# Kernel optimization log

Hardware: AMD Instinct MI355X
Metric: run time of the kernel (lower is better)

The kernel has to match this reference:

```python
import jax, jax.numpy as jnp
import numpy as np

BATCH, NUM_MASKS, IN_DIM, OUT_DIM = 512, 16, 1024, 1024


def setup_inputs() -> dict:
    key = jax.random.key(0)
    k1, k2, k3 = jax.random.split(key, 3)
    x = jax.random.normal(k1, (BATCH, NUM_MASKS, IN_DIM), dtype=jnp.float32)
    kernel = jax.random.normal(k2, (IN_DIM, OUT_DIM), dtype=jnp.float32) * (1.0 / np.sqrt(IN_DIM))
    masks = jax.random.uniform(k3, (NUM_MASKS, IN_DIM, OUT_DIM), dtype=jnp.float32)
    return {"x": x, "kernel": kernel, "masks": masks}


def reference(x, kernel, masks):
    # masked_kernel[m, i, o] = kernel[i, o] * masks[m, i, o]
    masked_kernel = kernel[None, :, :] * masks  # (M, I, O)
    # Original tf.scan serializes batch; equivalent math is one batched einsum:
    # out[b, m, o] = sum_i x[b, m, i] * masked_kernel[m, i, o]
    # NOTE: the executed tf.scan path applies NO activation, so neither do we.
    out = jnp.einsum('bmi,mio->bmo', x, masked_kernel)  # (B, M, O)
    return out
```

## Files before the change

kernel.cpp:

```cpp
#include <hip/hip_runtime.h>
#include <hip/hip_bf16.h>


#define BATCH 512
#define NMASK 16
#define IN_D  1024
#define OUT_D 1024

using bf16x8 = __attribute__((ext_vector_type(8))) __bf16;
using bf16x4 = __attribute__((ext_vector_type(4))) __bf16;
using f32x16 = __attribute__((ext_vector_type(16))) float;
using f32x4  = __attribute__((ext_vector_type(4))) float;
using f32x2  = __attribute__((ext_vector_type(2))) float;

typedef const __attribute__((address_space(1))) void gvoid_t;
typedef __attribute__((address_space(3))) void lvoid_t;

__device__ __forceinline__ void dma16(const void* g, const void* l) {
    __builtin_amdgcn_global_load_lds((gvoid_t*)(uintptr_t)g,
                                     (lvoid_t*)(uintptr_t)l, 16, 0, 0);
}

__global__ void __launch_bounds__(512, 4)
mdl_prep(const float* __restrict__ X,
         const float* __restrict__ Kn,
         const float* __restrict__ Mk,
         unsigned short* __restrict__ Wt,
         unsigned short* __restrict__ Xp)
{
    const int t   = threadIdx.x;
    const int bid = blockIdx.x;

    if (bid < 1024) {
        const int wg = (bid & 7) * 128 + (bid >> 3);
        const int m  = wg >> 6;
        const int G2 = wg & 63;
        const int g01 = t >> 8;
        const int oc  = t & 255;
        const int col0 = oc * 4;
        const int G = G2 * 2 + g01;
        const int i0 = G * 8;

        const float* mkb = Mk + ((size_t)m * IN_D + i0) * OUT_D + col0;
        const float* knb = Kn + (size_t)i0 * OUT_D + col0;

        f32x4 a[8], b[8];
#pragma unroll
        for (int r = 0; r < 8; ++r) {
            a[r] = *(const f32x4*)(mkb + (size_t)r * OUT_D);
            b[r] = *(const f32x4*)(knb + (size_t)r * OUT_D);
        }
        unsigned short* dst =
            Wt + (((size_t)m * 128 + G) * 1024 + col0) * 8;
#pragma unroll
        for (int c = 0; c < 4; ++c) {
            bf16x8 g;
#pragma unroll
            for (int r = 0; r < 8; ++r)
                g[r] = (__bf16)(a[r][c] * b[r][c]);
            *(bf16x8*)(dst + c * 8) = g;
        }
    } else {
        const int b2    = bid - 1024;
        const int strip = b2 >> 2;
        const int Gq    = b2 & 3;
        const int m  = strip >> 3;
        const int bt = strip & 7;
        const int row = t >> 3;
        const int oc  = t & 7;

        const float* src = X + ((size_t)(bt * 64 + row) * NMASK + m) * IN_D
                             + Gq * 256 + oc * 32;
        f32x4 av[8];
#pragma unroll
        for (int q = 0; q < 8; ++q)
            av[q] = *(const f32x4*)(src + q * 4);

        unsigned short* dstS = Xp + (size_t)strip * 65536
                                  + (size_t)(Gq * 32 + oc * 4) * 512 + row * 8;
#pragma unroll
        for (int j = 0; j < 4; ++j) {
            bf16x8 g;
#pragma unroll
            for (int e = 0; e < 4; ++e) {
                g[e]     = (__bf16)av[2 * j][e];
                g[4 + e] = (__bf16)av[2 * j + 1][e];
            }
            *(bf16x8*)(dstS + (size_t)j * 512) = g;
        }
    }
}

struct Frags { bf16x8 a[2][2]; bf16x8 b[2][2]; };

__global__ void __launch_bounds__(256, 2)
mdl_gemm2(const unsigned short* __restrict__ Xp,
          const unsigned short* __restrict__ Wt,
          float* __restrict__ Out)
{
    const int t = threadIdx.x;
    const int l = t & 63;
    const int w = t >> 6;

    const int raw = blockIdx.x;
    const int wg  = (raw & 7) * 64 + (raw >> 3);
    const int v   = wg * 4 + w;
    const int m   = v >> 7;
    const int v7  = v & 127;
    const int bt  = v7 >> 4;
    const int ot  = v7 & 15;

    const unsigned short* Ap = Xp + (size_t)(m * 8 + bt) * 65536;
    const int la = (l & 31) * 8;
    const int ls = l >> 5;
    const int bcol = ot * 64 + (l & 31);

    f32x16 acc[2][2];
#pragma unroll
    for (int ti = 0; ti < 2; ++ti)
#pragma unroll
        for (int tj = 0; tj < 2; ++tj)
#pragma unroll
            for (int e = 0; e < 16; ++e)
                acc[ti][tj][e] = 0.f;

    auto LOADF = [&](Frags& F, int kb) {
#pragma unroll
        for (int s = 0; s < 2; ++s) {
            const int G = (kb >> 3) + s * 2 + ls;
            const unsigned short* ab = Ap + (size_t)G * 512 + la;
            F.a[s][0] = *(const bf16x8*)(ab);
            F.a[s][1] = *(const bf16x8*)(ab + 256);
            const unsigned short* bb =
                Wt + (((size_t)m * 128 + G) * 1024 + bcol) * 8;
            F.b[s][0] = *(const bf16x8*)(bb);
            F.b[s][1] = *(const bf16x8*)(bb + 256);
        }
    };
    auto MF = [&](Frags& F) {
#pragma unroll
        for (int s = 0; s < 2; ++s)
#pragma unroll
            for (int ti = 0; ti < 2; ++ti)
#pragma unroll
                for (int tj = 0; tj < 2; ++tj)
                    acc[ti][tj] = __builtin_amdgcn_mfma_f32_32x32x16_bf16(
                        F.a[s][ti], F.b[s][tj], acc[ti][tj], 0, 0, 0);
    };

    Frags S0, S1;
    LOADF(S0, 0);
    for (int kb = 0; kb < IN_D; kb += 64) {
        LOADF(S1, kb + 32);
        __builtin_amdgcn_sched_barrier(0);
        MF(S0);
        LOADF(S0, (kb + 64) & (IN_D - 1));
        __builtin_amdgcn_sched_barrier(0);
        MF(S1);
    }

    const int r0 = bt * 64 + 4 * ls;
    const int c0 = ot * 64 + (l & 31);
#pragma unroll
    for (int ti = 0; ti < 2; ++ti) {
#pragma unroll
        for (int tj = 0; tj < 2; ++tj) {
#pragma unroll
            for (int g = 0; g < 4; ++g) {
#pragma unroll
                for (int q = 0; q < 4; ++q) {
                    const int row = r0 + ti * 32 + g * 8 + q;
                    const int col = c0 + tj * 32;
                    Out[((size_t)row * NMASK + m) * OUT_D + col] =
                        acc[ti][tj][g * 4 + q];
                }
            }
        }
    }
}

#define FAKP 40
#define FBKP 34
#define FMFSZ (32 * 128)

__global__ void __launch_bounds__(512, 4)
mdl_fused_fallback(const float* __restrict__ X,
                   const float* __restrict__ Kn,
                   const float* __restrict__ Mk,
                   float* __restrict__ Out)
{
    __shared__ __align__(16) float          Mf[3 * FMFSZ];
    __shared__ __align__(16) unsigned short As[128 * FAKP];
    __shared__ __align__(16) unsigned short Bs[128 * FBKP];

    const int t = threadIdx.x;
    const int l = t & 63;
    const int w = t >> 6;

    const int raw = blockIdx.x;
    const int wg  = (raw & 7) * 64 + (raw >> 3);
    const int m   = wg >> 5;
    const int ob  = (wg >> 2) & 7;
    const int bb  = wg & 3;

    const int wr = w >> 2, wc = w & 3;

    f32x4 acc[4][2];
#pragma unroll
    for (int mi = 0; mi < 4; ++mi)
#pragma unroll
        for (int ni = 0; ni < 2; ++ni)
            acc[mi][ni] = (f32x4){0.f, 0.f, 0.f, 0.f};

    const int a_row = t >> 2;
    const int a_kh  = (t & 3) * 8;
    const int o2 = (t & 63) * 2;
    const int k4 = w * 4;

    const int obase = ob * 128;
    const float* Xa  = X + ((size_t)(bb * 128 + a_row) * NMASK + m) * IN_D + a_kh;
    const float* Knb = Kn + obase + o2;
    const float* Mkm = Mk + (size_t)m * IN_D * OUT_D;

    auto DMA = [&](int tile, int c) {
        const int kt = tile * 32;
#pragma unroll
        for (int j = 0; j < 2; ++j) {
            const int k = j * 16 + w * 2 + (l >> 5);
            const float* gsrc = Mkm + (size_t)(kt + k) * OUT_D + obase + (l & 31) * 4;
            dma16(gsrc, &Mf[c * FMFSZ + j * 2048 + w * 256]);
        }
    };

    DMA(0, 0);
    DMA(1, 1);
    asm volatile("s_waitcnt vmcnt(2)" ::: "memory");
    __builtin_amdgcn_sched_barrier(0);
    __builtin_amdgcn_s_barrier();
    __builtin_amdgcn_sched_barrier(0);

    int c_cur = 0, c_nxt = 1, c_far = 2;

    for (int tt = 0; tt < 32; ++tt) {
        const int kt = tt * 32;
        f32x4 xv0 = *(const f32x4*)(Xa + kt);
        f32x4 xv1 = *(const f32x4*)(Xa + kt + 4);
        f32x2 kv[4];
#pragma unroll
        for (int r = 0; r < 4; ++r)
            kv[r] = *(const f32x2*)(Knb + (size_t)(kt + k4 + r) * OUT_D);
        __builtin_amdgcn_sched_barrier(0);
        DMA((tt + 2 < 32) ? tt + 2 : 0, c_far);
        __builtin_amdgcn_sched_barrier(0);
        {
            f32x2 mvv[4];
#pragma unroll
            for (int r = 0; r < 4; ++r)
                mvv[r] = *(const f32x2*)(&Mf[c_cur * FMFSZ + (k4 + r) * 128 + o2]);
#pragma unroll
            for (int c = 0; c < 2; ++c) {
                bf16x4 vv;
#pragma unroll
                for (int r = 0; r < 4; ++r)
                    vv[r] = (__bf16)(kv[r][c] * mvv[r][c]);
                *(bf16x4*)(&Bs[(o2 + c) * FBKP + k4]) = vv;
            }
            bf16x8 va;
#pragma unroll
            for (int j = 0; j < 4; ++j) {
                va[j] = (__bf16)xv0[j]; va[4 + j] = (__bf16)xv1[j];
            }
            *(bf16x8*)(&As[a_row * FAKP + a_kh]) = va;
        }
        asm volatile("s_waitcnt lgkmcnt(0)" ::: "memory");
        __builtin_amdgcn_sched_barrier(0);
        __builtin_amdgcn_s_barrier();
        __builtin_amdgcn_sched_barrier(0);
        {
            const int kg = (l >> 4) * 8;
            bf16x8 bfv[2];
#pragma unroll
            for (int ni = 0; ni < 2; ++ni) {
                const int n = wc * 32 + ni * 16 + (l & 15);
                bf16x4 lo = *(const bf16x4*)(&Bs[n * FBKP + kg]);
                bf16x4 hi = *(const bf16x4*)(&Bs[n * FBKP + kg + 4]);
                bf16x8 f;
                f[0] = lo[0]; f[1] = lo[1]; f[2] = lo[2]; f[3] = lo[3];
                f[4] = hi[0]; f[5] = hi[1]; f[6] = hi[2]; f[7] = hi[3];
                bfv[ni] = f;
            }
#pragma unroll
            for (int mi = 0; mi < 4; ++mi) {
                const int r = wr * 64 + mi * 16 + (l & 15);
                bf16x8 af = *(const bf16x8*)(&As[r * FAKP + kg]);
#pragma unroll
                for (int ni = 0; ni < 2; ++ni)
                    acc[mi][ni] = __builtin_amdgcn_mfma_f32_16x16x32_bf16(
                        af, bfv[ni], acc[mi][ni], 0, 0, 0);
            }
        }
        asm volatile("s_waitcnt vmcnt(2)" ::: "memory");
        __builtin_amdgcn_sched_barrier(0);
        __builtin_amdgcn_s_barrier();
        __builtin_amdgcn_sched_barrier(0);
        const int tmp = c_cur; c_cur = c_nxt; c_nxt = c_far; c_far = tmp;
    }
    asm volatile("s_waitcnt vmcnt(0)" ::: "memory");

    const int r0 = bb * 128 + wr * 64 + (l >> 4) * 4;
    const int c0 = ob * 128 + wc * 32 + (l & 15);
#pragma unroll
    for (int mi = 0; mi < 4; ++mi) {
#pragma unroll
        for (int j = 0; j < 4; ++j) {
            const size_t row = (size_t)(r0 + mi * 16 + j);
            float* op = Out + (row * NMASK + m) * OUT_D + c0;
#pragma unroll
            for (int ni = 0; ni < 2; ++ni)
                op[ni * 16] = acc[mi][ni][j];
        }
    }
}

extern "C" void kernel_launch(void* const* d_in, const int* in_sizes, int n_in,
                              void* d_out, int out_size, void* d_ws, size_t ws_size,
                              hipStream_t stream) {
    (void)in_sizes; (void)n_in; (void)out_size;
    const float* X  = (const float*)d_in[0];
    const float* Kn = (const float*)d_in[1];
    const float* Mk = (const float*)d_in[2];
    float* Out = (float*)d_out;

    const size_t w_bytes = (size_t)NMASK * IN_D * OUT_D * sizeof(unsigned short);
    const size_t x_bytes = (size_t)BATCH * NMASK * IN_D * sizeof(unsigned short);

    if (ws_size >= w_bytes + x_bytes) {
        unsigned short* Wt = (unsigned short*)d_ws;
        unsigned short* Xp = (unsigned short*)d_ws + w_bytes / 2;
        mdl_prep<<<1536, 512, 0, stream>>>(X, Kn, Mk, Wt, Xp);
        mdl_gemm2<<<512, 256, 0, stream>>>(Xp, Wt, Out);
    } else {
        mdl_fused_fallback<<<512, 512, 0, stream>>>(X, Kn, Mk, Out);
    }
}
```

Baseline: 60.86 us.

## Fuse X bf16 conversion into GEMM loads and simplify weight prep kernel

Drops the separate pass that converted X to a bf16 repacked buffer. The GEMM now reads fp32 X directly and converts it to bf16 fragments in registers. The weight prep kernel is rewritten with one column per thread, scalar loads and more, smaller blocks. This removes a 32MB fp32 read plus 16MB write pass over X, at the cost of reading X in fp32 (twice the bytes) inside the GEMM, with strided per-lane loads and possible re-reads across output tiles.

```diff
diff --git a/kernel.cpp b/kernel.cpp
--- a/kernel.cpp
+++ b/kernel.cpp
@@ -21,80 +21,40 @@
                                      (lvoid_t*)(uintptr_t)l, 16, 0, 0);
 }
 
-__global__ void __launch_bounds__(512, 4)
-mdl_prep(const float* __restrict__ X,
-         const float* __restrict__ Kn,
-         const float* __restrict__ Mk,
-         unsigned short* __restrict__ Wt,
-         unsigned short* __restrict__ Xp)
+__global__ void __launch_bounds__(256, 8)
+mdl_prep_w(const float* __restrict__ Kn,
+           const float* __restrict__ Mk,
+           unsigned short* __restrict__ Wt)
 {
-    const int t   = threadIdx.x;
-    const int bid = blockIdx.x;
-
-    if (bid < 1024) {
-        const int wg = (bid & 7) * 128 + (bid >> 3);
-        const int m  = wg >> 6;
-        const int G2 = wg & 63;
-        const int g01 = t >> 8;
-        const int oc  = t & 255;
-        const int col0 = oc * 4;
-        const int G = G2 * 2 + g01;
-        const int i0 = G * 8;
-
-        const float* mkb = Mk + ((size_t)m * IN_D + i0) * OUT_D + col0;
-        const float* knb = Kn + (size_t)i0 * OUT_D + col0;
-
-        f32x4 a[8], b[8];
-#pragma unroll
-        for (int r = 0; r < 8; ++r) {
-            a[r] = *(const f32x4*)(mkb + (size_t)r * OUT_D);
-            b[r] = *(const f32x4*)(knb + (size_t)r * OUT_D);
-        }
-        unsigned short* dst =
-            Wt + (((size_t)m * 128 + G) * 1024 + col0) * 8;
-#pragma unroll
-        for (int c = 0; c < 4; ++c) {
-            bf16x8 g;
-#pragma unroll
-            for (int r = 0; r < 8; ++r)
-                g[r] = (__bf16)(a[r][c] * b[r][c]);
-            *(bf16x8*)(dst + c * 8) = g;
-        }
-    } else {
-        const int b2    = bid - 1024;
-        const int strip = b2 >> 2;
-        const int Gq    = b2 & 3;
-        const int m  = strip >> 3;
-        const int bt = strip & 7;
-        const int row = t >> 3;
-        const int oc  = t & 7;
-
-        const float* src = X + ((size_t)(bt * 64 + row) * NMASK + m) * IN_D
-                             + Gq * 256 + oc * 32;
-        f32x4 av[8];
-#pragma unroll
-        for (int q = 0; q < 8; ++q)
-            av[q] = *(const f32x4*)(src + q * 4);
-
-        unsigned short* dstS = Xp + (size_t)strip * 65536
-                                  + (size_t)(Gq * 32 + oc * 4) * 512 + row * 8;
-#pragma unroll
-        for (int j = 0; j < 4; ++j) {
-            bf16x8 g;
-#pragma unroll
-            for (int e = 0; e < 4; ++e) {
-                g[e]     = (__bf16)av[2 * j][e];
-                g[4 + e] = (__bf16)av[2 * j + 1][e];
-            }
-            *(bf16x8*)(dstS + (size_t)j * 512) = g;
-        }
-    }
+    const int raw = blockIdx.x;
+    const int wg  = (raw & 7) * 1024 + (raw >> 3);
+    const int m  = wg >> 9;
+    const int G  = (wg >> 2) & 127;
+    const int cq = wg & 3;
+    const int col = cq * 256 + threadIdx.x;
+    const int i0  = G * 8;
+
+    const float* mk = Mk + ((size_t)m * IN_D + i0) * OUT_D + col;
+    const float* kn = Kn + (size_t)i0 * OUT_D + col;
+
+    float a[8], b[8];
+#pragma unroll
+    for (int r = 0; r < 8; ++r) {
+        a[r] = mk[(size_t)r * OUT_D];
+        b[r] = kn[(size_t)r * OUT_D];
+    }
+    bf16x8 g;
+#pragma unroll
+    for (int r = 0; r < 8; ++r)
+        g[r] = (__bf16)(a[r] * b[r]);
+
+    *(bf16x8*)(Wt + (((size_t)m * 128 + G) * 1024 + col) * 8) = g;
 }
 
 struct Frags { bf16x8 a[2][2]; bf16x8 b[2][2]; };
 
 __global__ void __launch_bounds__(256, 2)
-mdl_gemm2(const unsigned short* __restrict__ Xp,
+mdl_gemm2(const float* __restrict__ X,
           const unsigned short* __restrict__ Wt,
           float* __restrict__ Out)
 {
@@ -110,11 +70,11 @@
     const int bt  = v7 >> 4;
     const int ot  = v7 & 15;
 
-    const unsigned short* Ap = Xp + (size_t)(m * 8 + bt) * 65536;
-    const int la = (l & 31) * 8;
     const int ls = l >> 5;
     const int bcol = ot * 64 + (l & 31);
 
+    const float* Xb = X + ((size_t)(bt * 64 + (l & 31)) * NMASK + m) * IN_D;
+
     f32x16 acc[2][2];
 #pragma unroll
     for (int ti = 0; ti < 2; ++ti)
@@ -128,9 +88,19 @@
 #pragma unroll
         for (int s = 0; s < 2; ++s) {
             const int G = (kb >> 3) + s * 2 + ls;
-            const unsigned short* ab = Ap + (size_t)G * 512 + la;
-            F.a[s][0] = *(const bf16x8*)(ab);
-            F.a[s][1] = *(const bf16x8*)(ab + 256);
+#pragma unroll
+            for (int ti = 0; ti < 2; ++ti) {
+                const float* ap = Xb + (size_t)ti * (32 * NMASK * IN_D) + G * 8;
+                f32x4 x0 = *(const f32x4*)(ap);
+                f32x4 x1 = *(const f32x4*)(ap + 4);
+                bf16x8 af;
+#pragma unroll
+                for (int j = 0; j < 4; ++j) {
+                    af[j]     = (__bf16)x0[j];
+                    af[4 + j] = (__bf16)x1[j];
+                }
+                F.a[s][ti] = af;
+            }
             const unsigned short* bb =
                 Wt + (((size_t)m * 128 + G) * 1024 + bcol) * 8;
             F.b[s][0] = *(const bf16x8*)(bb);
@@ -332,13 +302,11 @@
     float* Out = (float*)d_out;
 
     const size_t w_bytes = (size_t)NMASK * IN_D * OUT_D * sizeof(unsigned short);
-    const size_t x_bytes = (size_t)BATCH * NMASK * IN_D * sizeof(unsigned short);
-
-    if (ws_size >= w_bytes + x_bytes) {
+
+    if (ws_size >= w_bytes) {
         unsigned short* Wt = (unsigned short*)d_ws;
-        unsigned short* Xp = (unsigned short*)d_ws + w_bytes / 2;
-        mdl_prep<<<1536, 512, 0, stream>>>(X, Kn, Mk, Wt, Xp);
-        mdl_gemm2<<<512, 256, 0, stream>>>(Xp, Wt, Out);
+        mdl_prep_w<<<8192, 256, 0, stream>>>(Kn, Mk, Wt);
+        mdl_gemm2<<<512, 256, 0, stream>>>(X, Wt, Out);
     } else {
         mdl_fused_fallback<<<512, 512, 0, stream>>>(X, Kn, Mk, Out);
     }
```

After: 98.53 us. +61.9%, slower.
